# Kernel tuning notes

Measured on AMD Instinct MI355X. Metric: run time of the kernel, lower is better.

## Reference

```python
import jax, jax.numpy as jnp
import numpy as np

B, T, L, D, K = 8, 16, 1024, 256, 128  # batch, temporal_shift, tokens/frame, hidden, top-k


def setup_inputs() -> dict:
    key = jax.random.key(0)
    ks = jax.random.split(key, 10)
    s1 = 1.0 / np.sqrt(D).astype(np.float32)
    s2 = 1.0 / np.sqrt(2 * D).astype(np.float32)
    return {
        "x": jax.random.normal(ks[0], (B, T, L, D), jnp.float32),
        "w_q_sig": jax.random.normal(ks[1], (D,), jnp.float32) * s1,
        "w_k_sig": jax.random.normal(ks[2], (D,), jnp.float32) * s1,
        "W_enc": jax.random.normal(ks[3], (2 * D, D), jnp.float32) * s2,
        "b_enc": jnp.zeros((D,), jnp.float32),
        "W_q": jax.random.normal(ks[4], (D, D), jnp.float32) * s1,
        "W_k": jax.random.normal(ks[5], (2 * D, D), jnp.float32) * s2,
        "W_v": jax.random.normal(ks[6], (2 * D, D), jnp.float32) * s2,
        "W_out": jax.random.normal(ks[7], (D, D), jnp.float32) * s1,
        "b_out": jnp.zeros((D,), jnp.float32),
    }


def reference(x, w_q_sig, w_k_sig, W_enc, b_enc, W_q, W_k, W_v, W_out, b_out):
    d = x.shape[-1]
    inv_sqrt_d = 1.0 / jnp.sqrt(jnp.asarray(d, x.dtype))

    # --- temporal-shifted attention signal: score each token against the
    # previous frame's tokens (temporal shift of 1 frame), pick top-k ---
    q_sig = jnp.einsum('btld,d->btl', x, w_q_sig)
    k_sig = jnp.einsum('btld,d->btl', jnp.roll(x, 1, axis=1), w_k_sig)
    attn = q_sig * k_sig * inv_sqrt_d                      # [B,T,L]
    idx = jax.lax.top_k(attn, K)[1]                        # [B,T,K] int32
    sel = jnp.take_along_axis(x, idx[..., None], axis=2)   # [B,T,K,D] selected tokens

    # --- kalman gain net: small encoder + cross-attention decoder ---
    def gain_net(enc_in, dec_kv):
        # enc_in, dec_kv: [B,K,2D]
        h = jax.nn.gelu(enc_in @ W_enc + b_enc)            # [B,K,D]
        qh = h @ W_q
        kh = dec_kv @ W_k
        vh = dec_kv @ W_v
        scores = jnp.einsum('bnd,bmd->bnm', qh, kh) * inv_sqrt_d
        ctx = jnp.einsum('bnm,bmd->bnd', jax.nn.softmax(scores, axis=-1), vh)
        return jax.nn.sigmoid(ctx @ W_out + b_out)         # [B,K,D] gain in (0,1)

    # --- sequential Kalman recurrence over T (faithful to kalman_step) ---
    def step(carry, xs):
        vel, prev_innov, prev_sud = carry
        prev_assoc, obs = xs
        pred = prev_assoc + vel
        innov = obs - pred
        state_evol_diff = pred - prev_assoc
        evol_diff = innov - prev_innov
        enc_in = jnp.concatenate([innov, state_evol_diff], axis=-1)
        dec_kv = jnp.concatenate([evol_diff, prev_sud], axis=-1)
        Kg = gain_net(enc_in, dec_kv)
        x_post = pred + Kg * innov
        sud = x_post - pred
        new_vel = x_post - prev_assoc
        return (new_vel, innov, sud), x_post

    z = jnp.zeros_like(sel[:, 0])
    xs = (jnp.swapaxes(sel[:, :-1], 0, 1), jnp.swapaxes(sel[:, 1:], 0, 1))
    _, posts = jax.lax.scan(step, (z, z, z), xs)           # [T-1,B,K,D]
    posts = jnp.swapaxes(posts, 0, 1)
    return jnp.concatenate([sel[:, :1], posts], axis=1)    # [B,T,K,D]
```

## Files before the change

kernel.cpp:

```cpp
#include <hip/hip_runtime.h>

#define NBT   128

__device__ __forceinline__ float4 ld4(const float* p) { return *(const float4*)p; }

__device__ __forceinline__ int selOff(int r, int t) {
  return (((r >> 7) * 16 + t) * 128 + (r & 127)) * 256;
}


__global__ __launch_bounds__(256) void sig_kernel(const float* __restrict__ x,
    const float* __restrict__ wq, const float* __restrict__ wk,
    float* __restrict__ sq, float* __restrict__ sk) {
  int tid = threadIdx.x;
  int row = blockIdx.x * 4 + (tid >> 6);
  int lane = tid & 63;
  float4 xv = ld4(x + (size_t)row * 256 + lane * 4);
  float4 a = ld4(wq + lane * 4);
  float4 b = ld4(wk + lane * 4);
  float dq = xv.x * a.x + xv.y * a.y + xv.z * a.z + xv.w * a.w;
  float dk = xv.x * b.x + xv.y * b.y + xv.z * b.z + xv.w * b.w;
  #pragma unroll
  for (int o = 32; o > 0; o >>= 1) {
    dq += __shfl_xor(dq, o, 64);
    dk += __shfl_xor(dk, o, 64);
  }
  if (lane == 0) { sq[row] = dq; sk[row] = dk; }
}

__global__ __launch_bounds__(256) void topk_kernel(const float* __restrict__ sq,
    const float* __restrict__ sk, int* __restrict__ idx) {
  __shared__ unsigned long long keys[1024];
  int bt = blockIdx.x;
  int t = bt & 15;
  int tp = (t + 15) & 15;
  const float* q = sq + bt * 1024;
  const float* kk = sk + (bt - t + tp) * 1024;
  for (int l = threadIdx.x; l < 1024; l += 256) {
    float v = q[l] * kk[l];
    unsigned u = __float_as_uint(v);
    unsigned s = (u & 0x80000000u) ? ~u : (u | 0x80000000u);
    keys[l] = ((unsigned long long)(~s) << 32) | (unsigned long long)l;
  }
  __syncthreads();
  for (int k = 2; k <= 1024; k <<= 1) {
    for (int j = k >> 1; j > 0; j >>= 1) {
      #pragma unroll
      for (int base = 0; base < 1024; base += 256) {
        int i = base + threadIdx.x;
        int ixj = i ^ j;
        if (ixj > i) {
          unsigned long long a = keys[i], b = keys[ixj];
          bool up = ((i & k) == 0);
          if ((a > b) == up) { keys[i] = b; keys[ixj] = a; }
        }
      }
      __syncthreads();
    }
  }
  if (threadIdx.x < 128)
    idx[bt * 128 + threadIdx.x] = (int)(keys[threadIdx.x] & 0xffffffffu);
}

__global__ __launch_bounds__(256) void gather_kernel(const float* __restrict__ x,
    const int* __restrict__ idx, float* __restrict__ sel, float* __restrict__ out) {
  int tid = threadIdx.x;
  int row = blockIdx.x * 4 + (tid >> 6);
  int lane = tid & 63;
  int bt = row >> 7;
  int j = idx[row];
  float4 v = ld4(x + ((size_t)bt * 1024 + j) * 256 + lane * 4);
  *(float4*)(sel + (size_t)row * 256 + lane * 4) = v;
  if ((bt & 15) == 0)
    *(float4*)(out + (size_t)row * 256 + lane * 4) = v;
}

__global__ __launch_bounds__(256) void stepA_kernel(
    const float* __restrict__ sel, const float* __restrict__ vel,
    const float* __restrict__ pinn, const float* __restrict__ psud,
    const float* __restrict__ W_enc, const float* __restrict__ b_enc,
    const float* __restrict__ W_q, const float* __restrict__ W_k,
    const float* __restrict__ W_v,
    float* __restrict__ qh, float* __restrict__ kh, float* __restrict__ vh, int t) {
  __shared__ float A[8][512];
  int tid = threadIdx.x;
  bool enc = blockIdx.x < 128;
  int r0 = (blockIdx.x & 127) * 8;

  {
    int rr = tid >> 5;
    int r = r0 + rr;
    int c = (tid & 31) * 4;
    #pragma unroll
    for (int p = 0; p < 2; ++p) {
      int cc = c + p * 128;
      float4 ob = ld4(sel + selOff(r, t) + cc);
      float4 pa = ld4(sel + selOff(r, t - 1) + cc);
      float4 ve = make_float4(0.f, 0.f, 0.f, 0.f);
      if (t > 1) ve = ld4(vel + r * 256 + cc);
      float4 in4;
      in4.x = ob.x - (pa.x + ve.x); in4.y = ob.y - (pa.y + ve.y);
      in4.z = ob.z - (pa.z + ve.z); in4.w = ob.w - (pa.w + ve.w);
      if (enc) {
        *(float4*)&A[rr][cc] = in4;
        *(float4*)&A[rr][256 + cc] = ve;
      } else {
        float4 dv = in4, ps = make_float4(0.f, 0.f, 0.f, 0.f);
        if (t > 1) {
          float4 pi = ld4(pinn + r * 256 + cc);
          ps = ld4(psud + r * 256 + cc);
          dv.x -= pi.x; dv.y -= pi.y; dv.z -= pi.z; dv.w -= pi.w;
        }
        *(float4*)&A[rr][cc] = dv;
        *(float4*)&A[rr][256 + cc] = ps;
      }
    }
  }
  __syncthreads();
  int rg = tid >> 6;
  int c4 = (tid & 63) * 4;
  if (enc) {
    float acc0[4] = {0,0,0,0}, acc1[4] = {0,0,0,0};
    for (int k = 0; k < 512; k += 4) {
      float4 a0 = *(const float4*)&A[rg * 2][k];
      float4 a1 = *(const float4*)&A[rg * 2 + 1][k];
      const float* a0p = (const float*)&a0;
      const float* a1p = (const float*)&a1;
      #pragma unroll
      for (int kk = 0; kk < 4; ++kk) {
        float4 w = ld4(W_enc + (k + kk) * 256 + c4);
        float x0 = a0p[kk], x1 = a1p[kk];
        acc0[0] += x0 * w.x; acc0[1] += x0 * w.y; acc0[2] += x0 * w.z; acc0[3] += x0 * w.w;
        acc1[0] += x1 * w.x; acc1[1] += x1 * w.y; acc1[2] += x1 * w.z; acc1[3] += x1 * w.w;
      }
    }
    float4 be = ld4(b_enc + c4);
    const float* bep = (const float*)&be;
    float h0[4], h1[4];
    #pragma unroll
    for (int i = 0; i < 4; ++i) {
      float v0 = acc0[i] + bep[i];
      float v1 = acc1[i] + bep[i];
      float u0 = 0.7978845608028654f * (v0 + 0.044715f * v0 * v0 * v0);
      float u1 = 0.7978845608028654f * (v1 + 0.044715f * v1 * v1 * v1);
      h0[i] = 0.5f * v0 * (1.f + tanhf(u0));
      h1[i] = 0.5f * v1 * (1.f + tanhf(u1));
    }
    __syncthreads();
    *(float4*)&A[rg * 2][c4] = *(float4*)h0;
    *(float4*)&A[rg * 2 + 1][c4] = *(float4*)h1;
    __syncthreads();
    float q0[4] = {0,0,0,0}, q1[4] = {0,0,0,0};
    for (int k = 0; k < 256; k += 4) {
      float4 a0 = *(const float4*)&A[rg * 2][k];
      float4 a1 = *(const float4*)&A[rg * 2 + 1][k];
      const float* a0p = (const float*)&a0;
      const float* a1p = (const float*)&a1;
      #pragma unroll
      for (int kk = 0; kk < 4; ++kk) {
        float4 w = ld4(W_q + (k + kk) * 256 + c4);
        float x0 = a0p[kk], x1 = a1p[kk];
        q0[0] += x0 * w.x; q0[1] += x0 * w.y; q0[2] += x0 * w.z; q0[3] += x0 * w.w;
        q1[0] += x1 * w.x; q1[1] += x1 * w.y; q1[2] += x1 * w.z; q1[3] += x1 * w.w;
      }
    }
    *(float4*)(qh + (r0 + rg * 2) * 256 + c4) = *(float4*)q0;
    *(float4*)(qh + (r0 + rg * 2 + 1) * 256 + c4) = *(float4*)q1;
  } else {
    float k0[4] = {0,0,0,0}, k1[4] = {0,0,0,0}, v0[4] = {0,0,0,0}, v1[4] = {0,0,0,0};
    for (int k = 0; k < 512; k += 4) {
      float4 a0 = *(const float4*)&A[rg * 2][k];
      float4 a1 = *(const float4*)&A[rg * 2 + 1][k];
      const float* a0p = (const float*)&a0;
      const float* a1p = (const float*)&a1;
      #pragma unroll
      for (int kk = 0; kk < 4; ++kk) {
        float4 wk4 = ld4(W_k + (k + kk) * 256 + c4);
        float4 wv4 = ld4(W_v + (k + kk) * 256 + c4);
        float x0 = a0p[kk], x1 = a1p[kk];
        k0[0] += x0 * wk4.x; k0[1] += x0 * wk4.y; k0[2] += x0 * wk4.z; k0[3] += x0 * wk4.w;
        k1[0] += x1 * wk4.x; k1[1] += x1 * wk4.y; k1[2] += x1 * wk4.z; k1[3] += x1 * wk4.w;
        v0[0] += x0 * wv4.x; v0[1] += x0 * wv4.y; v0[2] += x0 * wv4.z; v0[3] += x0 * wv4.w;
        v1[0] += x1 * wv4.x; v1[1] += x1 * wv4.y; v1[2] += x1 * wv4.z; v1[3] += x1 * wv4.w;
      }
    }
    *(float4*)(kh + (r0 + rg * 2) * 256 + c4) = *(float4*)k0;
    *(float4*)(kh + (r0 + rg * 2 + 1) * 256 + c4) = *(float4*)k1;
    *(float4*)(vh + (r0 + rg * 2) * 256 + c4) = *(float4*)v0;
    *(float4*)(vh + (r0 + rg * 2 + 1) * 256 + c4) = *(float4*)v1;
  }
}

__global__ __launch_bounds__(256) void stepBC_kernel(const float* __restrict__ qh,
    const float* __restrict__ khg, const float* __restrict__ vhg,
    const float* __restrict__ W_out, const float* __restrict__ b_out,
    const float* __restrict__ sel, float* __restrict__ vel,
    float* __restrict__ pinn, float* __restrict__ psud,
    float* __restrict__ out, int t) {
  __shared__ float q_lds[8][256];
  __shared__ float kh_t[32][260];
  __shared__ float P[8][128];
  int tid = threadIdx.x;
  int bb = blockIdx.x >> 4;
  int rg = blockIdx.x & 15;
  int r0 = bb * 128 + rg * 8;
  {
    int rr = tid >> 5;
    int c = (tid & 31) * 4;
    #pragma unroll
    for (int p = 0; p < 2; ++p) {
      int cc = c + p * 128;
      *(float4*)&q_lds[rr][cc] = ld4(qh + (r0 + rr) * 256 + cc);
    }
  }
  int r = tid >> 5;
  int mm = tid & 31;
  float s[4];
  for (int mt = 0; mt < 4; ++mt) {
    if (mt) __syncthreads();
    {
      int mi = tid >> 3;
      int cb = (tid & 7) * 4;
      const float* src = khg + (bb * 128 + mt * 32 + mi) * 256;
      #pragma unroll
      for (int p = 0; p < 8; ++p) {
        int cc = cb + p * 32;
        *(float4*)&kh_t[mi][cc] = ld4(src + cc);
      }
    }
    __syncthreads();
    float acc = 0.f;
    for (int k = 0; k < 256; k += 4) {
      float4 qv = *(const float4*)&q_lds[r][k];
      float4 kv = *(const float4*)&kh_t[mm][k];
      acc += qv.x * kv.x + qv.y * kv.y + qv.z * kv.z + qv.w * kv.w;
    }
    s[mt] = acc * 0.0625f;
  }
  float mx = fmaxf(fmaxf(s[0], s[1]), fmaxf(s[2], s[3]));
  #pragma unroll
  for (int o = 16; o > 0; o >>= 1) mx = fmaxf(mx, __shfl_xor(mx, o, 64));
  float e0 = expf(s[0] - mx), e1 = expf(s[1] - mx), e2 = expf(s[2] - mx), e3 = expf(s[3] - mx);
  float sum = e0 + e1 + e2 + e3;
  #pragma unroll
  for (int o = 16; o > 0; o >>= 1) sum += __shfl_xor(sum, o, 64);
  float inv = 1.f / sum;
  P[r][mm]      = e0 * inv;
  P[r][32 + mm] = e1 * inv;
  P[r][64 + mm] = e2 * inv;
  P[r][96 + mm] = e3 * inv;
  __syncthreads();
  int c8 = mm * 8;
  float a[8] = {0,0,0,0,0,0,0,0};
  const float* vb = vhg + bb * 128 * 256;
  for (int m = 0; m < 128; ++m) {
    float p = P[r][m];
    float4 va = ld4(vb + m * 256 + c8);
    float4 vc = ld4(vb + m * 256 + c8 + 4);
    a[0] += p * va.x; a[1] += p * va.y; a[2] += p * va.z; a[3] += p * va.w;
    a[4] += p * vc.x; a[5] += p * vc.y; a[6] += p * vc.z; a[7] += p * vc.w;
  }
  *(float4*)&q_lds[r][c8]     = *(float4*)&a[0];
  *(float4*)&q_lds[r][c8 + 4] = *(float4*)&a[4];
  __syncthreads();
  int rr = tid >> 5;
  int cc = (tid & 31) * 8;
  float acc8[8] = {0,0,0,0,0,0,0,0};
  for (int k = 0; k < 256; k += 4) {
    float4 cv = *(const float4*)&q_lds[rr][k];
    const float* cp = (const float*)&cv;
    #pragma unroll
    for (int kk = 0; kk < 4; ++kk) {
      float4 w0 = ld4(W_out + (k + kk) * 256 + cc);
      float4 w1 = ld4(W_out + (k + kk) * 256 + cc + 4);
      float xv = cp[kk];
      acc8[0] += xv * w0.x; acc8[1] += xv * w0.y; acc8[2] += xv * w0.z; acc8[3] += xv * w0.w;
      acc8[4] += xv * w1.x; acc8[5] += xv * w1.y; acc8[6] += xv * w1.z; acc8[7] += xv * w1.w;
    }
  }
  int row = r0 + rr;
  #pragma unroll
  for (int p = 0; p < 2; ++p) {
    int cp4 = cc + p * 4;
    float4 bo = ld4(b_out + cp4);
    const float* bop = (const float*)&bo;
    float4 ob = ld4(sel + selOff(row, t) + cp4);
    float4 pa = ld4(sel + selOff(row, t - 1) + cp4);
    float4 ve = make_float4(0.f, 0.f, 0.f, 0.f);
    int off = row * 256 + cp4;
    if (t > 1) ve = ld4(vel + off);
    const float* obp = (const float*)&ob;
    const float* pap = (const float*)&pa;
    const float* vep = (const float*)&ve;
    float inn[4], upd[4], ov[4], nv[4];
    #pragma unroll
    for (int i = 0; i < 4; ++i) {
      float g = 1.f / (1.f + expf(-(acc8[p * 4 + i] + bop[i])));
      float pr = pap[i] + vep[i];
      float in_ = obp[i] - pr;
      float up = g * in_;
      inn[i] = in_; upd[i] = up;
      ov[i] = pr + up;
      nv[i] = vep[i] + up;
    }
    *(float4*)(out + selOff(row, t) + cp4) = *(float4*)ov;
    *(float4*)(pinn + off) = *(float4*)inn;
    *(float4*)(psud + off) = *(float4*)upd;
    *(float4*)(vel + off)  = *(float4*)nv;
  }
}

extern "C" void kernel_launch(void* const* d_in, const int* in_sizes, int n_in,
                              void* d_out, int out_size, void* d_ws, size_t ws_size,
                              hipStream_t stream) {
  const float* x      = (const float*)d_in[0];
  const float* wq_sig = (const float*)d_in[1];
  const float* wk_sig = (const float*)d_in[2];
  const float* W_enc  = (const float*)d_in[3];
  const float* b_enc  = (const float*)d_in[4];
  const float* W_q    = (const float*)d_in[5];
  const float* W_k    = (const float*)d_in[6];
  const float* W_v    = (const float*)d_in[7];
  const float* W_out  = (const float*)d_in[8];
  const float* b_out  = (const float*)d_in[9];
  float* out = (float*)d_out;

  float* ws = (float*)d_ws;
  float* sq   = ws;
  float* sk   = ws + 131072;
  float* sel  = ws + 262144;
  float* vel  = ws + 4456448;
  float* pinn = ws + 4718592;
  float* psud = ws + 4980736;
  float* qh   = ws + 5242880;
  float* kh   = ws + 5505024;
  float* vh   = ws + 5767168;
  int*   idx  = (int*)(ws + 6029312);

  sig_kernel<<<32768, 256, 0, stream>>>(x, wq_sig, wk_sig, sq, sk);
  topk_kernel<<<NBT, 256, 0, stream>>>(sq, sk, idx);
  gather_kernel<<<4096, 256, 0, stream>>>(x, idx, sel, out);
  for (int t = 1; t < 16; ++t) {
    stepA_kernel<<<256, 256, 0, stream>>>(sel, vel, pinn, psud, W_enc, b_enc,
                                          W_q, W_k, W_v, qh, kh, vh, t);
    stepBC_kernel<<<128, 256, 0, stream>>>(qh, kh, vh, W_out, b_out, sel,
                                           vel, pinn, psud, out, t);
  }
}
```

Before: 2.011 ms.

## Stage stepA weight tiles into LDS with async double-buffered global_load_lds

The stepA GEMMs now copy weight tiles (W_enc, W_q, W_k/W_v) into a double-buffered LDS area with the direct global-to-LDS load builtin, prefetching the next tile while the current one is consumed. The thread mapping changes from four row-pairs across 64 columns to four threads per column group, each covering one row pair, so all four waves read the shared tile. The goal is to stop each wave fetching the same weights from global/L2 separately and to overlap the fetch with the FMAs. In exchange it adds a __syncthreads per K-tile and 32KB more LDS per block. The code relies on the builtin's per-lane LDS placement and has no explicit vmcnt wait before the barriers, so correctness depends on the compiler's waitcnt handling.

```diff
diff --git a/kernel.cpp b/kernel.cpp
--- a/kernel.cpp
+++ b/kernel.cpp
@@ -6,6 +6,32 @@
 
 __device__ __forceinline__ int selOff(int r, int t) {
   return (((r >> 7) * 16 + t) * 128 + (r & 127)) * 256;
+}
+
+__device__ __forceinline__ void stage16k(const float* g, float* l, int tid) {
+  int wave = tid >> 6, lane = tid & 63;
+  #pragma unroll
+  for (int c = 0; c < 4; ++c) {
+    int off = c * 4096 + wave * 1024;
+    __builtin_amdgcn_global_load_lds(
+        (const __attribute__((address_space(1))) void*)((const char*)g + off + lane * 16),
+        (__attribute__((address_space(3))) void*)((char*)l + off),
+        16, 0, 0);
+  }
+}
+
+__device__ __forceinline__ void stage_dec(const float* wk, const float* wv, float* db, int tid) {
+  int wave = tid >> 6, lane = tid & 63;
+  #pragma unroll
+  for (int i = 0; i < 2; ++i) {
+    int row = wave * 2 + i;
+    __builtin_amdgcn_global_load_lds(
+        (const __attribute__((address_space(1))) void*)(wk + row * 256 + lane * 4),
+        (__attribute__((address_space(3))) void*)(db + row * 512), 16, 0, 0);
+    __builtin_amdgcn_global_load_lds(
+        (const __attribute__((address_space(1))) void*)(wv + row * 256 + lane * 4),
+        (__attribute__((address_space(3))) void*)(db + row * 512 + 256), 16, 0, 0);
+  }
 }
 
 
@@ -82,7 +108,8 @@
     const float* __restrict__ W_q, const float* __restrict__ W_k,
     const float* __restrict__ W_v,
     float* __restrict__ qh, float* __restrict__ kh, float* __restrict__ vh, int t) {
-  __shared__ float A[8][512];
+  __shared__ __align__(16) float A[8][512];
+  __shared__ __align__(16) float WB[2][4096];
   int tid = threadIdx.x;
   bool enc = blockIdx.x < 128;
   int r0 = (blockIdx.x & 127) * 8;
@@ -116,23 +143,33 @@
       }
     }
   }
-  __syncthreads();
-  int rg = tid >> 6;
-  int c4 = (tid & 63) * 4;
+
+  int rp = tid & 3;
+  int r0l = 2 * rp;
+  int c4 = (tid >> 2) * 4;
+
   if (enc) {
+    stage16k(W_enc, WB[0], tid);
+    __syncthreads();
     float acc0[4] = {0,0,0,0}, acc1[4] = {0,0,0,0};
-    for (int k = 0; k < 512; k += 4) {
-      float4 a0 = *(const float4*)&A[rg * 2][k];
-      float4 a1 = *(const float4*)&A[rg * 2 + 1][k];
-      const float* a0p = (const float*)&a0;
-      const float* a1p = (const float*)&a1;
+    for (int kt = 0; kt < 32; ++kt) {
+      if (kt + 1 < 32) stage16k(W_enc + (kt + 1) * 4096, WB[(kt + 1) & 1], tid);
+      const float* wt = WB[kt & 1];
       #pragma unroll
-      for (int kk = 0; kk < 4; ++kk) {
-        float4 w = ld4(W_enc + (k + kk) * 256 + c4);
-        float x0 = a0p[kk], x1 = a1p[kk];
-        acc0[0] += x0 * w.x; acc0[1] += x0 * w.y; acc0[2] += x0 * w.z; acc0[3] += x0 * w.w;
-        acc1[0] += x1 * w.x; acc1[1] += x1 * w.y; acc1[2] += x1 * w.z; acc1[3] += x1 * w.w;
-      }
+      for (int kk = 0; kk < 16; kk += 4) {
+        float4 a0 = *(const float4*)&A[r0l][kt * 16 + kk];
+        float4 a1 = *(const float4*)&A[r0l + 1][kt * 16 + kk];
+        const float* a0p = (const float*)&a0;
+        const float* a1p = (const float*)&a1;
+        #pragma unroll
+        for (int j = 0; j < 4; ++j) {
+          float4 w = *(const float4*)&wt[(kk + j) * 256 + c4];
+          float x0 = a0p[j], x1 = a1p[j];
+          acc0[0] += x0 * w.x; acc0[1] += x0 * w.y; acc0[2] += x0 * w.z; acc0[3] += x0 * w.w;
+          acc1[0] += x1 * w.x; acc1[1] += x1 * w.y; acc1[2] += x1 * w.z; acc1[3] += x1 * w.w;
+        }
+      }
+      __syncthreads();
     }
     float4 be = ld4(b_enc + c4);
     const float* bep = (const float*)&be;
@@ -146,48 +183,63 @@
       h0[i] = 0.5f * v0 * (1.f + tanhf(u0));
       h1[i] = 0.5f * v1 * (1.f + tanhf(u1));
     }
-    __syncthreads();
-    *(float4*)&A[rg * 2][c4] = *(float4*)h0;
-    *(float4*)&A[rg * 2 + 1][c4] = *(float4*)h1;
+    *(float4*)&A[r0l][c4]     = *(float4*)h0;
+    *(float4*)&A[r0l + 1][c4] = *(float4*)h1;
+    stage16k(W_q, WB[0], tid);
     __syncthreads();
     float q0[4] = {0,0,0,0}, q1[4] = {0,0,0,0};
-    for (int k = 0; k < 256; k += 4) {
-      float4 a0 = *(const float4*)&A[rg * 2][k];
-      float4 a1 = *(const float4*)&A[rg * 2 + 1][k];
-      const float* a0p = (const float*)&a0;
-      const float* a1p = (const float*)&a1;
+    for (int kt = 0; kt < 16; ++kt) {
+      if (kt + 1 < 16) stage16k(W_q + (kt + 1) * 4096, WB[(kt + 1) & 1], tid);
+      const float* wt = WB[kt & 1];
       #pragma unroll
-      for (int kk = 0; kk < 4; ++kk) {
-        float4 w = ld4(W_q + (k + kk) * 256 + c4);
-        float x0 = a0p[kk], x1 = a1p[kk];
-        q0[0] += x0 * w.x; q0[1] += x0 * w.y; q0[2] += x0 * w.z; q0[3] += x0 * w.w;
-        q1[0] += x1 * w.x; q1[1] += x1 * w.y; q1[2] += x1 * w.z; q1[3] += x1 * w.w;
-      }
-    }
-    *(float4*)(qh + (r0 + rg * 2) * 256 + c4) = *(float4*)q0;
-    *(float4*)(qh + (r0 + rg * 2 + 1) * 256 + c4) = *(float4*)q1;
+      for (int kk = 0; kk < 16; kk += 4) {
+        float4 a0 = *(const float4*)&A[r0l][kt * 16 + kk];
+        float4 a1 = *(const float4*)&A[r0l + 1][kt * 16 + kk];
+        const float* a0p = (const float*)&a0;
+        const float* a1p = (const float*)&a1;
+        #pragma unroll
+        for (int j = 0; j < 4; ++j) {
+          float4 w = *(const float4*)&wt[(kk + j) * 256 + c4];
+          float x0 = a0p[j], x1 = a1p[j];
+          q0[0] += x0 * w.x; q0[1] += x0 * w.y; q0[2] += x0 * w.z; q0[3] += x0 * w.w;
+          q1[0] += x1 * w.x; q1[1] += x1 * w.y; q1[2] += x1 * w.z; q1[3] += x1 * w.w;
+        }
+      }
+      __syncthreads();
+    }
+    *(float4*)(qh + (r0 + r0l) * 256 + c4)     = *(float4*)q0;
+    *(float4*)(qh + (r0 + r0l + 1) * 256 + c4) = *(float4*)q1;
   } else {
+    stage_dec(W_k, W_v, WB[0], tid);
+    __syncthreads();
     float k0[4] = {0,0,0,0}, k1[4] = {0,0,0,0}, v0[4] = {0,0,0,0}, v1[4] = {0,0,0,0};
-    for (int k = 0; k < 512; k += 4) {
-      float4 a0 = *(const float4*)&A[rg * 2][k];
-      float4 a1 = *(const float4*)&A[rg * 2 + 1][k];
-      const float* a0p = (const float*)&a0;
-      const float* a1p = (const float*)&a1;
+    for (int kt = 0; kt < 64; ++kt) {
+      if (kt + 1 < 64)
+        stage_dec(W_k + (kt + 1) * 2048, W_v + (kt + 1) * 2048, WB[(kt + 1) & 1], tid);
+      const float* db = WB[kt & 1];
       #pragma unroll
-      for (int kk = 0; kk < 4; ++kk) {
-        float4 wk4 = ld4(W_k + (k + kk) * 256 + c4);
-        float4 wv4 = ld4(W_v + (k + kk) * 256 + c4);
-        float x0 = a0p[kk], x1 = a1p[kk];
-        k0[0] += x0 * wk4.x; k0[1] += x0 * wk4.y; k0[2] += x0 * wk4.z; k0[3] += x0 * wk4.w;
-        k1[0] += x1 * wk4.x; k1[1] += x1 * wk4.y; k1[2] += x1 * wk4.z; k1[3] += x1 * wk4.w;
-        v0[0] += x0 * wv4.x; v0[1] += x0 * wv4.y; v0[2] += x0 * wv4.z; v0[3] += x0 * wv4.w;
-        v1[0] += x1 * wv4.x; v1[1] += x1 * wv4.y; v1[2] += x1 * wv4.z; v1[3] += x1 * wv4.w;
-      }
-    }
-    *(float4*)(kh + (r0 + rg * 2) * 256 + c4) = *(float4*)k0;
-    *(float4*)(kh + (r0 + rg * 2 + 1) * 256 + c4) = *(float4*)k1;
-    *(float4*)(vh + (r0 + rg * 2) * 256 + c4) = *(float4*)v0;
-    *(float4*)(vh + (r0 + rg * 2 + 1) * 256 + c4) = *(float4*)v1;
+      for (int kk = 0; kk < 8; kk += 4) {
+        float4 a0 = *(const float4*)&A[r0l][kt * 8 + kk];
+        float4 a1 = *(const float4*)&A[r0l + 1][kt * 8 + kk];
+        const float* a0p = (const float*)&a0;
+        const float* a1p = (const float*)&a1;
+        #pragma unroll
+        for (int j = 0; j < 4; ++j) {
+          float4 wk4 = *(const float4*)&db[(kk + j) * 512 + c4];
+          float4 wv4 = *(const float4*)&db[(kk + j) * 512 + 256 + c4];
+          float x0 = a0p[j], x1 = a1p[j];
+          k0[0] += x0 * wk4.x; k0[1] += x0 * wk4.y; k0[2] += x0 * wk4.z; k0[3] += x0 * wk4.w;
+          k1[0] += x1 * wk4.x; k1[1] += x1 * wk4.y; k1[2] += x1 * wk4.z; k1[3] += x1 * wk4.w;
+          v0[0] += x0 * wv4.x; v0[1] += x0 * wv4.y; v0[2] += x0 * wv4.z; v0[3] += x0 * wv4.w;
+          v1[0] += x1 * wv4.x; v1[1] += x1 * wv4.y; v1[2] += x1 * wv4.z; v1[3] += x1 * wv4.w;
+        }
+      }
+      __syncthreads();
+    }
+    *(float4*)(kh + (r0 + r0l) * 256 + c4)     = *(float4*)k0;
+    *(float4*)(kh + (r0 + r0l + 1) * 256 + c4) = *(float4*)k1;
+    *(float4*)(vh + (r0 + r0l) * 256 + c4)     = *(float4*)v0;
+    *(float4*)(vh + (r0 + r0l + 1) * 256 + c4) = *(float4*)v1;
   }
 }
 
```

Measured after the change: 1.757 ms. 1.14x faster.
